# Kernel tuning notes

Measured on AMD Instinct MI355X. Metric: run time of the kernel, lower is better.

The kernel has to match this reference:

```python
import jax, jax.numpy as jnp
import numpy as np

# Equal-sized graph batches (batch vectors are sorted, contiguous segments)
B, NX, NY = 16, 1024, 4096   # clouds, coarse pts/cloud, fine pts/cloud
C, CS, H = 256, 128, 256     # coarse feat dim, skip feat dim, MLP hidden
EPS = 1e-8


def setup_inputs() -> dict:
    key = jax.random.key(0)
    ks = jax.random.split(key, 8)
    x = jax.random.normal(ks[0], (B * NX, C), dtype=jnp.float32)
    pos = jax.random.normal(ks[1], (B * NX, 3), dtype=jnp.float32)
    x_skip = jax.random.normal(ks[2], (B * NY, CS), dtype=jnp.float32)
    pos_skip = jax.random.normal(ks[3], (B * NY, 3), dtype=jnp.float32)
    batch = jnp.repeat(jnp.arange(B, dtype=jnp.int32), NX)
    batch_skip = jnp.repeat(jnp.arange(B, dtype=jnp.int32), NY)
    W1 = jax.random.normal(ks[4], (C + CS, H), dtype=jnp.float32) * 0.05
    b1 = jnp.zeros((H,), dtype=jnp.float32)
    W2 = jax.random.normal(ks[5], (H, H), dtype=jnp.float32) * 0.05
    b2 = jnp.zeros((H,), dtype=jnp.float32)
    return {"x": x, "pos": pos, "batch": batch, "x_skip": x_skip,
            "pos_skip": pos_skip, "batch_skip": batch_skip,
            "W1": W1, "b1": b1, "W2": W2, "b2": b2, "k": 3}


def knn_interpolate(x, pos, pos_skip, k):
    # Reshape flat batched point sets into [B, n, .] (batch vectors are
    # contiguous equal-sized segments, so this matches the per-batch loop).
    fx = x.reshape(B, NX, C)
    px = pos.reshape(B, NX, 3)
    py = pos_skip.reshape(B, NY, 3)
    # Squared distances via the Gram trick: [B, NY, NX]
    d2 = (jnp.sum(py * py, -1)[:, :, None]
          + jnp.sum(px * px, -1)[:, None, :]
          - 2.0 * jnp.einsum('byd,bxd->byx', py, px))
    neg_d2, idx = jax.lax.top_k(-d2, k)            # k nearest (smallest d2)
    dist = jnp.sqrt(jnp.maximum(-neg_d2, 0.0))     # [B, NY, k]
    w = 1.0 / (dist + EPS)
    gathered = jax.vmap(lambda f, i: f[i])(fx, idx)  # [B, NY, k, C]
    num = jnp.einsum('byk,bykc->byc', w, gathered)
    den = jnp.sum(w, axis=-1, keepdims=True) + EPS
    return (num / den).reshape(B * NY, C)


def reference(x, pos, batch, x_skip, pos_skip, batch_skip, W1, b1, W2, b2, k):
    interp = knn_interpolate(x, pos, pos_skip, k)      # [B*NY, C]
    h = jnp.concatenate([interp, x_skip], axis=1)      # [B*NY, C+CS]
    h = jax.nn.relu(h @ W1 + b1)
    h = jax.nn.relu(h @ W2 + b2)
    return h
```

## Files before the change

kernel.cpp:

```cpp
#include <hip/hip_runtime.h>
#include <hip/hip_bf16.h>

#define B_  16
#define NX_ 1024
#define NY_ 4096
#define C_  256
#define CS_ 128
#define H_  256
#define M_  (B_ * NY_)
#define K1_ (C_ + CS_)
#define K2_ (H_)

using short8  = __attribute__((ext_vector_type(8))) short;
using floatx4 = __attribute__((ext_vector_type(4))) float;

__device__ __forceinline__ unsigned short f2bf(float f) {
    unsigned int u = __float_as_uint(f);
    unsigned int r = (u + 0x7fffu + ((u >> 16) & 1u)) >> 16;
    return (unsigned short)r;
}

typedef const __attribute__((address_space(1))) void gas_t;
typedef __attribute__((address_space(3))) void las_t;
__device__ __forceinline__ void gload_lds16(const void* g, void* l) {
    __builtin_amdgcn_global_load_lds((gas_t*)g, (las_t*)l, 16, 0, 0);
}

__global__ __launch_bounds__(256) void knn_select(
    const float* __restrict__ pos, const float* __restrict__ pos_skip,
    int4* __restrict__ idx4, float4* __restrict__ wgt4)
{
    __shared__ float4 sp[NX_];
    __shared__ float  md[7][3][32];
    __shared__ int    mi[7][3][32];

    const int tid = threadIdx.x;
    const int e   = tid >> 5;
    const int p   = tid & 31;
    const int y   = blockIdx.x * 32 + p;
    const int b   = y >> 12;

    for (int j = tid; j < NX_; j += 256) {
        const float* pp = pos + (size_t)(b * NX_ + j) * 3;
        float px = pp[0], py = pp[1], pz = pp[2];
        float pn = __fadd_rn(__fadd_rn(__fmul_rn(px, px), __fmul_rn(py, py)),
                             __fmul_rn(pz, pz));
        sp[j] = make_float4(px, py, pz, pn);
    }
    __syncthreads();

    const float* qp = pos_skip + (size_t)y * 3;
    const float qx = qp[0], qy = qp[1], qz = qp[2];
    const float qn = __fadd_rn(__fadd_rn(__fmul_rn(qx, qx), __fmul_rn(qy, qy)),
                               __fmul_rn(qz, qz));

    float d0 = 3.4e38f, d1 = 3.4e38f, d2 = 3.4e38f;
    int   n0 = 0x7fffffff, n1 = 0x7fffffff, n2 = 0x7fffffff;
    const int j0 = e * 128;
    #pragma unroll 8
    for (int t = 0; t < 128; ++t) {
        const int j = j0 + t;
        const float4 pv = sp[j];
        float dot = __fadd_rn(__fadd_rn(__fmul_rn(qx, pv.x),
                                        __fmul_rn(qy, pv.y)),
                              __fmul_rn(qz, pv.z));
        float dd = __fsub_rn(__fadd_rn(qn, pv.w), __fmul_rn(2.0f, dot));
        if (dd < d2) {
            if (dd < d1) {
                d2 = d1; n2 = n1;
                if (dd < d0) { d1 = d0; n1 = n0; d0 = dd; n0 = j; }
                else         { d1 = dd; n1 = j; }
            } else { d2 = dd; n2 = j; }
        }
    }

    if (e != 0) {
        md[e - 1][0][p] = d0; md[e - 1][1][p] = d1; md[e - 1][2][p] = d2;
        mi[e - 1][0][p] = n0; mi[e - 1][1][p] = n1; mi[e - 1][2][p] = n2;
    }
    __syncthreads();

    if (e == 0) {
        #pragma unroll
        for (int m = 0; m < 7; ++m) {
            const float b0 = md[m][0][p], b1 = md[m][1][p], b2 = md[m][2][p];
            const int  ib0 = mi[m][0][p], ib1 = mi[m][1][p], ib2 = mi[m][2][p];
            const float a0 = d0, a1 = d1, a2 = d2;
            const int  ia0 = n0, ia1 = n1, ia2 = n2;
            if (a0 <= b0) {
                d0 = a0; n0 = ia0;
                if (a1 <= b0) { d1 = a1; n1 = ia1;
                    bool c = (a2 <= b0); d2 = c ? a2 : b0; n2 = c ? ia2 : ib0; }
                else          { d1 = b0; n1 = ib0;
                    bool c = (a1 <= b1); d2 = c ? a1 : b1; n2 = c ? ia1 : ib1; }
            } else {
                d0 = b0; n0 = ib0;
                if (a0 <= b1) { d1 = a0; n1 = ia0;
                    bool c = (a1 <= b1); d2 = c ? a1 : b1; n2 = c ? ia1 : ib1; }
                else          { d1 = b1; n1 = ib1;
                    bool c = (a0 <= b2); d2 = c ? a0 : b2; n2 = c ? ia0 : ib2; }
            }
        }
        const float w0 = 1.0f / (sqrtf(fmaxf(d0, 0.0f)) + 1e-8f);
        const float w1 = 1.0f / (sqrtf(fmaxf(d1, 0.0f)) + 1e-8f);
        const float w2 = 1.0f / (sqrtf(fmaxf(d2, 0.0f)) + 1e-8f);
        const float inv_den = 1.0f / (w0 + w1 + w2 + 1e-8f);
        idx4[y] = make_int4(n0, n1, n2, 0);
        wgt4[y] = make_float4(w0, w1, w2, inv_den);
    }
}

__global__ __launch_bounds__(256) void prep_w(
    const float* __restrict__ W1, const float* __restrict__ W2,
    unsigned short* __restrict__ W1t, unsigned short* __restrict__ W2t)
{
    int id = blockIdx.x * 256 + threadIdx.x;
    if (id < K1_ * H_) {
        int n = id / K1_, k = id - n * K1_;
        W1t[id] = f2bf(W1[(size_t)k * H_ + n]);
    }
    if (id < K2_ * H_) {
        int n = id >> 8, k = id & 255;
        W2t[id] = f2bf(W2[(size_t)k * H_ + n]);
    }
}

__global__ __launch_bounds__(256) void gemm1_fused(
    const float* __restrict__ x, const float* __restrict__ x_skip,
    const int4* __restrict__ idx4, const float4* __restrict__ wgt4,
    const unsigned short* __restrict__ Bt,
    const float* __restrict__ bias,
    unsigned short* __restrict__ outp)
{
    __shared__ unsigned short As_full[6 * 64 * 64];
    __shared__ unsigned short Bs[256 * 64];

    const int tid  = threadIdx.x;
    const int lane = tid & 63;
    const int wave = tid >> 6;
    const int m0   = blockIdx.x * 64;
    const int r16  = lane & 15, qk = lane >> 4;

    auto stageB = [&](int kt) {
        #pragma unroll
        for (int i = 0; i < 8; ++i) {
            const int row  = (tid >> 3) + i * 32;
            const int slot = (tid & 7) ^ (row & 7);
            gload_lds16(Bt + (size_t)row * K1_ + kt + slot * 8,
                        &Bs[row * 64 + (tid & 7) * 8]);
        }
    };

    stageB(0);

    {
        const int ks  = lane >> 4;
        const int cs  = (lane * 4) & 63;
        const int sl  = cs >> 3;
        const int of  = cs & 7;
        const int ks2  = 4 + (lane >> 5);
        const int cs2  = (lane * 2) & 63;
        const int sl2  = cs2 >> 3;
        const int of2  = cs2 & 7;
        #pragma unroll 4
        for (int i = 0; i < 16; ++i) {
            const int r  = wave * 16 + i;
            const int gr = m0 + r;
            const int4   id = idx4[gr];
            const float4 wt = wgt4[gr];
            const float* fb = x + (size_t)(gr >> 12) * (NX_ * C_);
            const float4 f0 = *(const float4*)(fb + (size_t)id.x * C_ + lane * 4);
            const float4 f1 = *(const float4*)(fb + (size_t)id.y * C_ + lane * 4);
            const float4 f2 = *(const float4*)(fb + (size_t)id.z * C_ + lane * 4);
            ushort4 o;
            o.x = f2bf((wt.x * f0.x + wt.y * f1.x + wt.z * f2.x) * wt.w);
            o.y = f2bf((wt.x * f0.y + wt.y * f1.y + wt.z * f2.y) * wt.w);
            o.z = f2bf((wt.x * f0.z + wt.y * f1.z + wt.z * f2.z) * wt.w);
            o.w = f2bf((wt.x * f0.w + wt.y * f1.w + wt.z * f2.w) * wt.w);
            *(ushort4*)&As_full[ks * 4096 + r * 64 + (sl ^ (r & 7)) * 8 + of] = o;

            const float2 s2 = *(const float2*)(x_skip + (size_t)gr * CS_ + lane * 2);
            ushort2 os; os.x = f2bf(s2.x); os.y = f2bf(s2.y);
            *(ushort2*)&As_full[ks2 * 4096 + r * 64 + (sl2 ^ (r & 7)) * 8 + of2] = os;
        }
    }
    __syncthreads();

    floatx4 acc[4][4] = {};

    #pragma unroll
    for (int t = 0; t < 6; ++t) {
        const unsigned short* At = As_full + t * 4096;
        #pragma unroll
        for (int s = 0; s < 2; ++s) {
            short8 af[4], bf[4];
            #pragma unroll
            for (int m = 0; m < 4; ++m) {
                const int row  = m * 16 + r16;
                const int slot = (s * 4 + qk) ^ (r16 & 7);
                af[m] = *(const short8*)&At[row * 64 + slot * 8];
            }
            #pragma unroll
            for (int n = 0; n < 4; ++n) {
                const int row  = wave * 64 + n * 16 + r16;
                const int slot = (s * 4 + qk) ^ (r16 & 7);
                bf[n] = *(const short8*)&Bs[row * 64 + slot * 8];
            }
            #pragma unroll
            for (int m = 0; m < 4; ++m)
                #pragma unroll
                for (int n = 0; n < 4; ++n)
                    acc[m][n] = __builtin_amdgcn_mfma_f32_16x16x32_bf16(
                        af[m], bf[n], acc[m][n], 0, 0, 0);
        }
        if (t < 5) {
            __syncthreads();
            stageB((t + 1) * 64);
            __syncthreads();
        }
    }

    #pragma unroll
    for (int n = 0; n < 4; ++n) {
        const int gc = wave * 64 + n * 16 + r16;
        const float bv = bias[gc];
        #pragma unroll
        for (int m = 0; m < 4; ++m) {
            #pragma unroll
            for (int r = 0; r < 4; ++r) {
                const int gr = m0 + m * 16 + qk * 4 + r;
                float v = fmaxf(acc[m][n][r] + bv, 0.0f);
                outp[(size_t)gr * H_ + gc] = f2bf(v);
            }
        }
    }
}

__global__ __launch_bounds__(256) void gemm2_bias_relu(
    const unsigned short* __restrict__ A,
    const unsigned short* __restrict__ Bt,
    const float* __restrict__ bias,
    float* __restrict__ outp)
{
    __shared__ unsigned short As[2][64 * 64];
    __shared__ unsigned short Bs[2][256 * 64];

    const int tid  = threadIdx.x;
    const int lane = tid & 63;
    const int wave = tid >> 6;
    const int m0   = blockIdx.x * 64;
    const int r16  = lane & 15, qk = lane >> 4;

    floatx4 acc[4][4] = {};

    auto stage = [&](int buf, int kt) {
        #pragma unroll
        for (int i = 0; i < 2; ++i) {
            const int row  = (tid >> 3) + i * 32;
            const int slot = (tid & 7) ^ (row & 7);
            gload_lds16(A + (size_t)(m0 + row) * K2_ + kt + slot * 8,
                        &As[buf][row * 64 + (tid & 7) * 8]);
        }
        #pragma unroll
        for (int i = 0; i < 8; ++i) {
            const int row  = (tid >> 3) + i * 32;
            const int slot = (tid & 7) ^ (row & 7);
            gload_lds16(Bt + (size_t)row * K2_ + kt + slot * 8,
                        &Bs[buf][row * 64 + (tid & 7) * 8]);
        }
    };

    auto compute = [&](int buf) {
        #pragma unroll
        for (int s = 0; s < 2; ++s) {
            short8 af[4], bf[4];
            #pragma unroll
            for (int m = 0; m < 4; ++m) {
                const int row  = m * 16 + r16;
                const int slot = (s * 4 + qk) ^ (r16 & 7);
                af[m] = *(const short8*)&As[buf][row * 64 + slot * 8];
            }
            #pragma unroll
            for (int n = 0; n < 4; ++n) {
                const int row  = wave * 64 + n * 16 + r16;
                const int slot = (s * 4 + qk) ^ (r16 & 7);
                bf[n] = *(const short8*)&Bs[buf][row * 64 + slot * 8];
            }
            #pragma unroll
            for (int m = 0; m < 4; ++m)
                #pragma unroll
                for (int n = 0; n < 4; ++n)
                    acc[m][n] = __builtin_amdgcn_mfma_f32_16x16x32_bf16(
                        af[m], bf[n], acc[m][n], 0, 0, 0);
        }
    };

    stage(0, 0);
    __syncthreads();
    int cur = 0;
    #pragma unroll
    for (int t = 1; t < 4; ++t) {
        stage(cur ^ 1, t * 64);
        compute(cur);
        __syncthreads();
        cur ^= 1;
    }
    compute(cur);

    #pragma unroll
    for (int n = 0; n < 4; ++n) {
        const int gc = wave * 64 + n * 16 + r16;
        const float bv = bias[gc];
        #pragma unroll
        for (int m = 0; m < 4; ++m) {
            #pragma unroll
            for (int r = 0; r < 4; ++r) {
                const int gr = m0 + m * 16 + qk * 4 + r;
                outp[(size_t)gr * H_ + gc] = fmaxf(acc[m][n][r] + bv, 0.0f);
            }
        }
    }
}

extern "C" void kernel_launch(void* const* d_in, const int* in_sizes, int n_in,
                              void* d_out, int out_size, void* d_ws, size_t ws_size,
                              hipStream_t stream)
{
    const float* x        = (const float*)d_in[0];
    const float* pos      = (const float*)d_in[1];
    const float* x_skip   = (const float*)d_in[3];
    const float* pos_skip = (const float*)d_in[4];
    const float* W1       = (const float*)d_in[6];
    const float* b1       = (const float*)d_in[7];
    const float* W2       = (const float*)d_in[8];
    const float* b2       = (const float*)d_in[9];

    char* ws = (char*)d_ws;
    unsigned short* h1  = (unsigned short*)(ws);
    unsigned short* W1t = (unsigned short*)(ws + 33554432);
    unsigned short* W2t = (unsigned short*)(ws + 33751040);
    int4*           idx4 = (int4*)(ws + 33882112);
    float4*         wgt4 = (float4*)(ws + 34930688);

    hipLaunchKernelGGL(knn_select, dim3(M_ / 32), dim3(256), 0, stream,
                       pos, pos_skip, idx4, wgt4);
    hipLaunchKernelGGL(prep_w, dim3((K1_ * H_ + 255) / 256), dim3(256), 0, stream,
                       W1, W2, W1t, W2t);
    hipLaunchKernelGGL(gemm1_fused, dim3(M_ / 64), dim3(256), 0, stream,
                       x, x_skip, idx4, wgt4, W1t, b1, h1);
    hipLaunchKernelGGL(gemm2_bias_relu, dim3(M_ / 64), dim3(256), 0, stream,
                       h1, W2t, b2, (float*)d_out);
}
```

Measured before the change: 206.8 us.

## Fold weight prep into knn kernel, remap gemm1 blocks, single-buffer gemm2

```diff
diff --git a/kernel.cpp b/kernel.cpp
--- a/kernel.cpp
+++ b/kernel.cpp
@@ -28,7 +28,9 @@
 
 __global__ __launch_bounds__(256) void knn_select(
     const float* __restrict__ pos, const float* __restrict__ pos_skip,
-    int4* __restrict__ idx4, float4* __restrict__ wgt4)
+    int4* __restrict__ idx4, float4* __restrict__ wgt4,
+    const float* __restrict__ W1, const float* __restrict__ W2,
+    unsigned short* __restrict__ W1t, unsigned short* __restrict__ W2t)
 {
     __shared__ float4 sp[NX_];
     __shared__ float  md[7][3][32];
@@ -39,6 +41,18 @@
     const int p   = tid & 31;
     const int y   = blockIdx.x * 32 + p;
     const int b   = y >> 12;
+
+    {
+        const int id = blockIdx.x * 256 + tid;
+        if (id < K1_ * H_) {
+            int n = id / K1_, k = id - n * K1_;
+            W1t[id] = f2bf(W1[(size_t)k * H_ + n]);
+        }
+        if (id < K2_ * H_) {
+            int n = id >> 8, k = id & 255;
+            W2t[id] = f2bf(W2[(size_t)k * H_ + n]);
+        }
+    }
 
     for (int j = tid; j < NX_; j += 256) {
         const float* pp = pos + (size_t)(b * NX_ + j) * 3;
@@ -110,22 +124,7 @@
     }
 }
 
-__global__ __launch_bounds__(256) void prep_w(
-    const float* __restrict__ W1, const float* __restrict__ W2,
-    unsigned short* __restrict__ W1t, unsigned short* __restrict__ W2t)
-{
-    int id = blockIdx.x * 256 + threadIdx.x;
-    if (id < K1_ * H_) {
-        int n = id / K1_, k = id - n * K1_;
-        W1t[id] = f2bf(W1[(size_t)k * H_ + n]);
-    }
-    if (id < K2_ * H_) {
-        int n = id >> 8, k = id & 255;
-        W2t[id] = f2bf(W2[(size_t)k * H_ + n]);
-    }
-}
-
-__global__ __launch_bounds__(256) void gemm1_fused(
+__global__ __launch_bounds__(256, 2) void gemm1_fused(
     const float* __restrict__ x, const float* __restrict__ x_skip,
     const int4* __restrict__ idx4, const float4* __restrict__ wgt4,
     const unsigned short* __restrict__ Bt,
@@ -138,7 +137,9 @@
     const int tid  = threadIdx.x;
     const int lane = tid & 63;
     const int wave = tid >> 6;
-    const int m0   = blockIdx.x * 64;
+    const int bid  = blockIdx.x;
+    const int lb   = (bid & 7) * 128 + (bid >> 3);
+    const int m0   = lb * 64;
     const int r16  = lane & 15, qk = lane >> 4;
 
     auto stageB = [&](int kt) {
@@ -162,26 +163,35 @@
         const int cs2  = (lane * 2) & 63;
         const int sl2  = cs2 >> 3;
         const int of2  = cs2 & 7;
-        #pragma unroll 4
-        for (int i = 0; i < 16; ++i) {
-            const int r  = wave * 16 + i;
-            const int gr = m0 + r;
-            const int4   id = idx4[gr];
-            const float4 wt = wgt4[gr];
-            const float* fb = x + (size_t)(gr >> 12) * (NX_ * C_);
-            const float4 f0 = *(const float4*)(fb + (size_t)id.x * C_ + lane * 4);
-            const float4 f1 = *(const float4*)(fb + (size_t)id.y * C_ + lane * 4);
-            const float4 f2 = *(const float4*)(fb + (size_t)id.z * C_ + lane * 4);
-            ushort4 o;
-            o.x = f2bf((wt.x * f0.x + wt.y * f1.x + wt.z * f2.x) * wt.w);
-            o.y = f2bf((wt.x * f0.y + wt.y * f1.y + wt.z * f2.y) * wt.w);
-            o.z = f2bf((wt.x * f0.z + wt.y * f1.z + wt.z * f2.z) * wt.w);
-            o.w = f2bf((wt.x * f0.w + wt.y * f1.w + wt.z * f2.w) * wt.w);
-            *(ushort4*)&As_full[ks * 4096 + r * 64 + (sl ^ (r & 7)) * 8 + of] = o;
-
-            const float2 s2 = *(const float2*)(x_skip + (size_t)gr * CS_ + lane * 2);
-            ushort2 os; os.x = f2bf(s2.x); os.y = f2bf(s2.y);
-            *(ushort2*)&As_full[ks2 * 4096 + r * 64 + (sl2 ^ (r & 7)) * 8 + of2] = os;
+        #pragma unroll
+        for (int batch = 0; batch < 2; ++batch) {
+            int4 ids[8]; float4 wts[8];
+            #pragma unroll
+            for (int i = 0; i < 8; ++i) {
+                const int gr = m0 + wave * 16 + batch * 8 + i;
+                ids[i] = idx4[gr];
+                wts[i] = wgt4[gr];
+            }
+            #pragma unroll
+            for (int i = 0; i < 8; ++i) {
+                const int r  = wave * 16 + batch * 8 + i;
+                const int gr = m0 + r;
+                const float4 wt = wts[i];
+                const float* fb = x + (size_t)(gr >> 12) * (NX_ * C_);
+                const float4 f0 = *(const float4*)(fb + (size_t)ids[i].x * C_ + lane * 4);
+                const float4 f1 = *(const float4*)(fb + (size_t)ids[i].y * C_ + lane * 4);
+                const float4 f2 = *(const float4*)(fb + (size_t)ids[i].z * C_ + lane * 4);
+                ushort4 o;
+                o.x = f2bf((wt.x * f0.x + wt.y * f1.x + wt.z * f2.x) * wt.w);
+                o.y = f2bf((wt.x * f0.y + wt.y * f1.y + wt.z * f2.y) * wt.w);
+                o.z = f2bf((wt.x * f0.z + wt.y * f1.z + wt.z * f2.z) * wt.w);
+                o.w = f2bf((wt.x * f0.w + wt.y * f1.w + wt.z * f2.w) * wt.w);
+                *(ushort4*)&As_full[ks * 4096 + r * 64 + (sl ^ (r & 7)) * 8 + of] = o;
+
+                const float2 s2 = *(const float2*)(x_skip + (size_t)gr * CS_ + lane * 2);
+                ushort2 os; os.x = f2bf(s2.x); os.y = f2bf(s2.y);
+                *(ushort2*)&As_full[ks2 * 4096 + r * 64 + (sl2 ^ (r & 7)) * 8 + of2] = os;
+            }
         }
     }
     __syncthreads();
@@ -236,14 +246,14 @@
     }
 }
 
-__global__ __launch_bounds__(256) void gemm2_bias_relu(
+__global__ __launch_bounds__(256, 4) void gemm2_bias_relu(
     const unsigned short* __restrict__ A,
     const unsigned short* __restrict__ Bt,
     const float* __restrict__ bias,
     float* __restrict__ outp)
 {
-    __shared__ unsigned short As[2][64 * 64];
-    __shared__ unsigned short Bs[2][256 * 64];
+    __shared__ unsigned short As[64 * 64];
+    __shared__ unsigned short Bs[256 * 64];
 
     const int tid  = threadIdx.x;
     const int lane = tid & 63;
@@ -253,24 +263,28 @@
 
     floatx4 acc[4][4] = {};
 
-    auto stage = [&](int buf, int kt) {
+    auto stage = [&](int kt) {
         #pragma unroll
         for (int i = 0; i < 2; ++i) {
             const int row  = (tid >> 3) + i * 32;
             const int slot = (tid & 7) ^ (row & 7);
             gload_lds16(A + (size_t)(m0 + row) * K2_ + kt + slot * 8,
-                        &As[buf][row * 64 + (tid & 7) * 8]);
+                        &As[row * 64 + (tid & 7) * 8]);
         }
         #pragma unroll
         for (int i = 0; i < 8; ++i) {
             const int row  = (tid >> 3) + i * 32;
             const int slot = (tid & 7) ^ (row & 7);
             gload_lds16(Bt + (size_t)row * K2_ + kt + slot * 8,
-                        &Bs[buf][row * 64 + (tid & 7) * 8]);
+                        &Bs[row * 64 + (tid & 7) * 8]);
         }
     };
 
-    auto compute = [&](int buf) {
+    #pragma unroll
+    for (int t = 0; t < 4; ++t) {
+        if (t) __syncthreads();
+        stage(t * 64);
+        __syncthreads();
         #pragma unroll
         for (int s = 0; s < 2; ++s) {
             short8 af[4], bf[4];
@@ -278,13 +292,13 @@
             for (int m = 0; m < 4; ++m) {
                 const int row  = m * 16 + r16;
                 const int slot = (s * 4 + qk) ^ (r16 & 7);
-                af[m] = *(const short8*)&As[buf][row * 64 + slot * 8];
+                af[m] = *(const short8*)&As[row * 64 + slot * 8];
             }
             #pragma unroll
             for (int n = 0; n < 4; ++n) {
                 const int row  = wave * 64 + n * 16 + r16;
                 const int slot = (s * 4 + qk) ^ (r16 & 7);
-                bf[n] = *(const short8*)&Bs[buf][row * 64 + slot * 8];
+                bf[n] = *(const short8*)&Bs[row * 64 + slot * 8];
             }
             #pragma unroll
             for (int m = 0; m < 4; ++m)
@@ -293,19 +307,7 @@
                     acc[m][n] = __builtin_amdgcn_mfma_f32_16x16x32_bf16(
                         af[m], bf[n], acc[m][n], 0, 0, 0);
         }
-    };
-
-    stage(0, 0);
-    __syncthreads();
-    int cur = 0;
-    #pragma unroll
-    for (int t = 1; t < 4; ++t) {
-        stage(cur ^ 1, t * 64);
-        compute(cur);
-        __syncthreads();
-        cur ^= 1;
-    }
-    compute(cur);
+    }
 
     #pragma unroll
     for (int n = 0; n < 4; ++n) {
@@ -343,9 +345,7 @@
     float4*         wgt4 = (float4*)(ws + 34930688);
 
     hipLaunchKernelGGL(knn_select, dim3(M_ / 32), dim3(256), 0, stream,
-                       pos, pos_skip, idx4, wgt4);
-    hipLaunchKernelGGL(prep_w, dim3((K1_ * H_ + 255) / 256), dim3(256), 0, stream,
-                       W1, W2, W1t, W2t);
+                       pos, pos_skip, idx4, wgt4, W1, W2, W1t, W2t);
     hipLaunchKernelGGL(gemm1_fused, dim3(M_ / 64), dim3(256), 0, stream,
                        x, x_skip, idx4, wgt4, W1t, b1, h1);
     hipLaunchKernelGGL(gemm2_bias_relu, dim3(M_ / 64), dim3(256), 0, stream,
```

Result: no change. 205.5 us (-0.6%).
